# Performance work log

Measured on AMD Instinct MI355X. Metric: run time of the kernel, lower is better.

## Reference

```python
import jax, jax.numpy as jnp
import numpy as np

EMBED_DIM = 1024
N_HEADS = 16
HEAD_DIM = EMBED_DIM // N_HEADS
B, T = 1, 4096

def setup_inputs() -> dict:
    key = jax.random.key(0)
    k1, k2, k3 = jax.random.split(key, 3)
    x = jax.random.normal(k1, (B, T, EMBED_DIM), dtype=jnp.float32)
    # match nn.Linear init scale roughly (not required for correctness testing)
    w_qkv = jax.random.normal(k2, (EMBED_DIM, 3 * EMBED_DIM), dtype=jnp.float32) * (EMBED_DIM ** -0.5)
    w_out = jax.random.normal(k3, (EMBED_DIM, EMBED_DIM), dtype=jnp.float32) * (EMBED_DIM ** -0.5)
    return {"x": x, "w_qkv": w_qkv, "w_out": w_out}

def reference(x, w_qkv, w_out):
    b, t, c = x.shape
    qkv = x @ w_qkv                                  # [B,T,3C]
    q, k, v = jnp.split(qkv, 3, axis=-1)
    # [B,T,C] -> [B,H,T,D]
    def heads(a):
        return a.reshape(b, t, N_HEADS, HEAD_DIM).transpose(0, 2, 1, 3)
    q, k, v = heads(q), heads(k), heads(v)
    scale = 1.0 / jnp.sqrt(jnp.asarray(HEAD_DIM, dtype=x.dtype))
    att = jnp.einsum('bhqd,bhkd->bhqk', q, k) * scale  # [B,H,T,T] (full matrix, as in source)
    att = jax.nn.softmax(att, axis=-1)
    y = jnp.einsum('bhqk,bhkd->bhqd', att, v)          # [B,H,T,D]
    y = y.transpose(0, 2, 1, 3).reshape(b, t, c)
    return y @ w_out
```

## Files before the change

kernel.cpp:

```cpp
#include <hip/hip_runtime.h>
#include <hip/hip_bf16.h>

#define T_SEQ 4096
#define C_DIM 1024
#define NH    16
#define HD    64
#define C3    3072

typedef __attribute__((ext_vector_type(8))) short short8;
typedef __attribute__((ext_vector_type(4))) short short4v;
typedef __attribute__((ext_vector_type(4))) float f32x4;
typedef __attribute__((ext_vector_type(16))) float f32x16;

__device__ __forceinline__ short f2bf(float f) {
  union { float f; unsigned u; } v; v.f = f;
  unsigned r = v.u + 0x7FFFu + ((v.u >> 16) & 1u);
  return (short)(r >> 16);
}

__device__ __forceinline__ unsigned cvt_pk_bf16(float lo, float hi) {
  unsigned r;
  asm volatile("v_cvt_pk_bf16_f32 %0, %1, %2" : "=v"(r) : "v"(lo), "v"(hi));
  return r;
}

__device__ __forceinline__ float exp2_fast(float x) {
  return __builtin_amdgcn_exp2f(x);
}

__device__ __forceinline__ float max_half64(float v) {
  return fmaxf(v, __shfl_xor(v, 32, 64));
}
__device__ __forceinline__ float sum_half64(float v) {
  return v + __shfl_xor(v, 32, 64);
}

__device__ __forceinline__ void gld_lds16(const void* g, void* l) {
  __builtin_amdgcn_global_load_lds(
      (const __attribute__((address_space(1))) unsigned int*)g,
      (__attribute__((address_space(3))) unsigned int*)l, 16, 0, 0);
}

__global__ __launch_bounds__(256) void conv_bf16_kernel(const float* __restrict__ in,
                                                        short* __restrict__ out) {
  const size_t i = ((size_t)blockIdx.x * 256 + threadIdx.x) * 8;
  float4 v0 = *(const float4*)(in + i);
  float4 v1 = *(const float4*)(in + i + 4);
  short8 o;
  o[0] = f2bf(v0.x); o[1] = f2bf(v0.y); o[2] = f2bf(v0.z); o[3] = f2bf(v0.w);
  o[4] = f2bf(v1.x); o[5] = f2bf(v1.y); o[6] = f2bf(v1.z); o[7] = f2bf(v1.w);
  *(short8*)(out + i) = o;
}

__global__ void trans_conv_kernel(const float* __restrict__ in, short* __restrict__ out,
                                  int K, int N) {
  __shared__ float t[32][33];
  const int n0 = blockIdx.x * 32, k0 = blockIdx.y * 32;
  const int tx = threadIdx.x, ty = threadIdx.y;
  for (int i = ty; i < 32; i += 8) t[i][tx] = in[(size_t)(k0 + i) * N + n0 + tx];
  __syncthreads();
  for (int i = ty; i < 32; i += 8) out[(size_t)(n0 + i) * K + k0 + tx] = f2bf(t[tx][i]);
}

__device__ __forceinline__ void store_out(short* C, size_t idx, float v) { C[idx] = f2bf(v); }
__device__ __forceinline__ void store_out(float* C, size_t idx, float v) { C[idx] = v; }

template <typename OutT>
__global__ __launch_bounds__(256) void gemm_bt_kernel(const short* __restrict__ A,
                                                      const short* __restrict__ BT,
                                                      OutT* __restrict__ C,
                                                      int M, int N, int K) {
  __shared__ __align__(16) short As[128 * 32];
  __shared__ __align__(16) short Bs[128 * 32];
  const int tid = threadIdx.x;
  const int wid = tid >> 6;
  const int lane = tid & 63;
  const int l15 = lane & 15;
  const int l4 = lane >> 4;
  const int wr = wid >> 1;
  const int wc = wid & 1;
  const int bm = blockIdx.y * 128;
  const int bn = blockIdx.x * 128;

  f32x4 acc[4][4];
#pragma unroll
  for (int m = 0; m < 4; ++m)
#pragma unroll
    for (int n = 0; n < 4; ++n) acc[m][n] = (f32x4){0.f, 0.f, 0.f, 0.f};

  const int ebase = wid * 1024;
  const int e0 = ebase + lane * 8;
  const int r0 = e0 >> 5, c0 = e0 & 31;
  const int r1 = r0 + 16;

  for (int k0 = 0; k0 < K; k0 += 32) {
    __syncthreads();
    gld_lds16(A + (size_t)(bm + r0) * K + k0 + c0, As + ebase);
    gld_lds16(A + (size_t)(bm + r1) * K + k0 + c0, As + ebase + 512);
    gld_lds16(BT + (size_t)(bn + r0) * K + k0 + c0, Bs + ebase);
    gld_lds16(BT + (size_t)(bn + r1) * K + k0 + c0, Bs + ebase + 512);
    __syncthreads();

    short8 a[4], b[4];
#pragma unroll
    for (int m = 0; m < 4; ++m)
      a[m] = *(const short8*)&As[(wr * 64 + m * 16 + l15) * 32 + l4 * 8];
#pragma unroll
    for (int n = 0; n < 4; ++n)
      b[n] = *(const short8*)&Bs[(wc * 64 + n * 16 + l15) * 32 + l4 * 8];
#pragma unroll
    for (int m = 0; m < 4; ++m)
#pragma unroll
      for (int n = 0; n < 4; ++n)
        acc[m][n] = __builtin_amdgcn_mfma_f32_16x16x32_bf16(a[m], b[n], acc[m][n], 0, 0, 0);
  }

#pragma unroll
  for (int m = 0; m < 4; ++m) {
    const int row0 = bm + wr * 64 + m * 16 + l4 * 4;
#pragma unroll
    for (int n = 0; n < 4; ++n) {
      const int col = bn + wc * 64 + n * 16 + l15;
#pragma unroll
      for (int r = 0; r < 4; ++r)
        store_out(C, (size_t)(row0 + r) * N + col, acc[m][n][r]);
    }
  }
}

__global__ __launch_bounds__(256) void repack_v_kernel(const short* __restrict__ qkv,
                                                       short* __restrict__ vT) {
  const int h = blockIdx.x >> 6;
  const int t0 = (blockIdx.x & 63) << 6;
  __shared__ __align__(16) short tile[64][72];
  const int t = threadIdx.x;
  const int r = t >> 3, c = (t & 7) << 3;
#pragma unroll
  for (int i = 0; i < 2; ++i) {
    const int rr = r + i * 32;
    *(short8*)&tile[rr][c] =
        *(const short8*)&qkv[(size_t)(t0 + rr) * C3 + 2048 + h * 64 + c];
  }
  __syncthreads();
  const int d = t >> 3, tt = (t & 7) << 3;
#pragma unroll
  for (int i = 0; i < 2; ++i) {
    const int dd = d + i * 32;
    short8 v;
#pragma unroll
    for (int j = 0; j < 8; ++j) v[j] = tile[tt + j][dd];
    *(short8*)&vT[(size_t)(h * 64 + dd) * T_SEQ + t0 + tt] = v;
  }
}

__global__ __launch_bounds__(512, 4) void attn_kernel(const short* __restrict__ qkv,
                                                      const short* __restrict__ vT,
                                                      short* __restrict__ y) {
  const int bid = blockIdx.x;
  const int xcd = bid & 7, slot = bid >> 3;
  const int h = xcd * 2 + (slot >> 5);
  const int q0 = (slot & 31) * 128;

  const int tid = threadIdx.x;
  const int w = tid >> 6, lane = tid & 63, l31 = lane & 31, l1 = lane >> 5;
  const int g = w >> 2, wg = w & 3;
  const int kvbase = g * (T_SEQ / 2);

  __shared__ __align__(16) short Ks[2][2][4096];
  __shared__ __align__(16) short Vs[2][2][4096];

  short8 qf[4];
  {
    const short* qp = qkv + (size_t)(q0 + wg * 32 + l31) * C3 + h * 64 + l1 * 8;
#pragma unroll
    for (int ks = 0; ks < 4; ++ks) qf[ks] = *(const short8*)(qp + ks * 16);
  }

  f32x16 oa0, oa1;
#pragma unroll
  for (int r = 0; r < 16; ++r) { oa0[r] = 0.f; oa1[r] = 0.f; }
  float m_r = -INFINITY, l_r = 0.f;
  const float SCL = 0.125f * 1.44269504f;
  const float TH = 8.0f / SCL;

  const int lr0 = wg * 8 + (lane >> 3);
  const int csw = ((lane & 7) << 3) ^ ((lane >> 3) << 3);
  const short* kgb = qkv + 1024 + h * 64 + csw;
  const short* vgb = vT + (size_t)(h * 64 + lr0) * T_SEQ + csw;
  const int rswz = (l31 & 7) << 3;

  auto stage = [&](int buf, int kv0) {
#pragma unroll
    for (int i = 0; i < 2; ++i) {
      gld_lds16(kgb + (size_t)(kv0 + lr0 + i * 32) * C3, &Ks[g][buf][i * 2048 + wg * 512]);
      gld_lds16(vgb + (size_t)(i * 32) * T_SEQ + kv0, &Vs[g][buf][i * 2048 + wg * 512]);
    }
  };

  stage(0, kvbase);

  const int NT = T_SEQ / 2 / 64;
  for (int t = 0; t < NT; ++t) {
    const int cur = t & 1;
    __syncthreads();
    if (t < NT - 1) stage(cur ^ 1, kvbase + (t + 1) * 64);

    const short* Kb = &Ks[g][cur][0];
    const short* Vb = &Vs[g][cur][0];

    f32x16 s0, s1;
#pragma unroll
    for (int r = 0; r < 16; ++r) { s0[r] = 0.f; s1[r] = 0.f; }
    __builtin_amdgcn_s_setprio(1);
#pragma unroll
    for (int ks = 0; ks < 4; ++ks) {
      const int c = (ks * 16 + l1 * 8) ^ rswz;
      short8 k0 = *(const short8*)&Kb[l31 * 64 + c];
      short8 k1 = *(const short8*)&Kb[(32 + l31) * 64 + c];
      s0 = __builtin_amdgcn_mfma_f32_32x32x16_bf16(k0, qf[ks], s0, 0, 0, 0);
      s1 = __builtin_amdgcn_mfma_f32_32x32x16_bf16(k1, qf[ks], s1, 0, 0, 0);
    }
    __builtin_amdgcn_s_setprio(0);

    float tm;
    {
      float t8[8];
#pragma unroll
      for (int r = 0; r < 8; ++r)
        t8[r] = fmaxf(fmaxf(s0[r], s0[r + 8]), fmaxf(s1[r], s1[r + 8]));
#pragma unroll
      for (int r = 0; r < 4; ++r) t8[r] = fmaxf(t8[r], t8[r + 4]);
      tm = fmaxf(fmaxf(t8[0], t8[2]), fmaxf(t8[1], t8[3]));
    }
    tm = max_half64(tm);

    if (__any(tm > m_r + TH)) {
      const float mn = fmaxf(m_r, tm);
      const float al = exp2_fast((m_r - mn) * SCL);
      m_r = mn;
      l_r *= al;
#pragma unroll
      for (int r = 0; r < 16; ++r) { oa0[r] *= al; oa1[r] *= al; }
    }
    const float msc = m_r * SCL;
#pragma unroll
    for (int r = 0; r < 16; ++r) s0[r] = exp2_fast(fmaf(s0[r], SCL, -msc));
#pragma unroll
    for (int r = 0; r < 16; ++r) s1[r] = exp2_fast(fmaf(s1[r], SCL, -msc));

    float ps;
    {
      float u8[8];
#pragma unroll
      for (int r = 0; r < 8; ++r)
        u8[r] = (s0[r] + s0[r + 8]) + (s1[r] + s1[r + 8]);
#pragma unroll
      for (int r = 0; r < 4; ++r) u8[r] += u8[r + 4];
      ps = (u8[0] + u8[2]) + (u8[1] + u8[3]);
    }
    ps = sum_half64(ps);
    l_r += ps;

    unsigned pw[4][4];
#pragma unroll
    for (int half = 0; half < 2; ++half) {
      const f32x16& sv = half ? s1 : s0;
#pragma unroll
      for (int kk = 0; kk < 2; ++kk) {
        const int ks = half * 2 + kk;
        unsigned x0 = cvt_pk_bf16(sv[kk * 8 + 0], sv[kk * 8 + 1]);
        unsigned y0 = cvt_pk_bf16(sv[kk * 8 + 4], sv[kk * 8 + 5]);
        asm volatile("s_nop 0\n\tv_permlane32_swap_b32 %0, %1" : "+v"(x0), "+v"(y0));
        unsigned x1 = cvt_pk_bf16(sv[kk * 8 + 2], sv[kk * 8 + 3]);
        unsigned y1 = cvt_pk_bf16(sv[kk * 8 + 6], sv[kk * 8 + 7]);
        asm volatile("s_nop 0\n\tv_permlane32_swap_b32 %0, %1" : "+v"(x1), "+v"(y1));
        pw[ks][0] = x0; pw[ks][1] = x1; pw[ks][2] = y0; pw[ks][3] = y1;
      }
    }

    __builtin_amdgcn_s_setprio(1);
#pragma unroll
    for (int ks = 0; ks < 4; ++ks) {
      union { unsigned u[4]; short8 s8; } uu;
      uu.u[0] = pw[ks][0]; uu.u[1] = pw[ks][1]; uu.u[2] = pw[ks][2]; uu.u[3] = pw[ks][3];
      const int c = (ks * 16 + l1 * 8) ^ rswz;
      short8 v0 = *(const short8*)&Vb[l31 * 64 + c];
      short8 v1 = *(const short8*)&Vb[(32 + l31) * 64 + c];
      oa0 = __builtin_amdgcn_mfma_f32_32x32x16_bf16(v0, uu.s8, oa0, 0, 0, 0);
      oa1 = __builtin_amdgcn_mfma_f32_32x32x16_bf16(v1, uu.s8, oa1, 0, 0, 0);
    }
    __builtin_amdgcn_s_setprio(0);
  }

  __syncthreads();
  float* Oex = (float*)&Vs[0][0][0];
  float* mex = (float*)&Ks[0][0][0];
  const int xslot = wg * 64 + lane;
  if (g == 1) {
#pragma unroll
    for (int r = 0; r < 16; ++r) {
      Oex[r * 256 + xslot] = oa0[r];
      Oex[(16 + r) * 256 + xslot] = oa1[r];
    }
    mex[xslot] = m_r;
    mex[256 + xslot] = l_r;
  }
  __syncthreads();
  if (g == 0) {
    const float m_b = mex[xslot], l_b = mex[256 + xslot];
    const float mm = fmaxf(m_r, m_b);
    const float a = exp2_fast((m_r - mm) * SCL);
    const float b = exp2_fast((m_b - mm) * SCL);
    const float rl = 1.0f / (l_r * a + l_b * b);
    const float ra = a * rl, rb = b * rl;
    const size_t yb = (size_t)(q0 + wg * 32 + l31) * C_DIM + h * 64;
#pragma unroll
    for (int g4 = 0; g4 < 4; ++g4) {
      short4v o0, o1;
#pragma unroll
      for (int j = 0; j < 4; ++j) {
        o0[j] = f2bf(oa0[g4 * 4 + j] * ra + Oex[(g4 * 4 + j) * 256 + xslot] * rb);
        o1[j] = f2bf(oa1[g4 * 4 + j] * ra + Oex[(16 + g4 * 4 + j) * 256 + xslot] * rb);
      }
      *(short4v*)&y[yb + g4 * 8 + l1 * 4] = o0;
      *(short4v*)&y[yb + 32 + g4 * 8 + l1 * 4] = o1;
    }
  }
}

extern "C" void kernel_launch(void* const* d_in, const int* in_sizes, int n_in,
                              void* d_out, int out_size, void* d_ws, size_t ws_size,
                              hipStream_t stream) {
  const float* x = (const float*)d_in[0];
  const float* w_qkv = (const float*)d_in[1];
  const float* w_out = (const float*)d_in[2];
  float* out = (float*)d_out;

  char* ws = (char*)d_ws;
  short* xb = (short*)ws;            ws += (size_t)T_SEQ * C_DIM * 2;
  short* wqT = (short*)ws;           ws += (size_t)C3 * C_DIM * 2;
  short* woT = (short*)ws;           ws += (size_t)C_DIM * C_DIM * 2;
  short* qkv = (short*)ws;           ws += (size_t)T_SEQ * C3 * 2;
  short* vT = (short*)ws;            ws += (size_t)NH * T_SEQ * HD * 2;
  short* y = (short*)ws;             ws += (size_t)T_SEQ * C_DIM * 2;

  conv_bf16_kernel<<<(T_SEQ * C_DIM) / (256 * 8), 256, 0, stream>>>(x, xb);
  trans_conv_kernel<<<dim3(C3 / 32, C_DIM / 32), dim3(32, 8), 0, stream>>>(w_qkv, wqT, C_DIM, C3);
  trans_conv_kernel<<<dim3(C_DIM / 32, C_DIM / 32), dim3(32, 8), 0, stream>>>(w_out, woT, C_DIM, C_DIM);

  gemm_bt_kernel<short><<<dim3(C3 / 128, T_SEQ / 128), 256, 0, stream>>>(xb, wqT, qkv,
                                                                         T_SEQ, C3, C_DIM);
  repack_v_kernel<<<NH * (T_SEQ / 64), 256, 0, stream>>>(qkv, vT);

  attn_kernel<<<512, 512, 0, stream>>>(qkv, vT, y);

  gemm_bt_kernel<float><<<dim3(C_DIM / 128, T_SEQ / 128), 256, 0, stream>>>(y, woT, out,
                                                                            T_SEQ, C_DIM, C_DIM);
}
```

Baseline: 182.3 us.

## Pipeline KV staging with explicit vmcnt waits and split barriers

Replaces the single __syncthreads with two raw s_barriers around the next-tile prefetch, and waits with vmcnt(4) so only the current tile's async global-to-LDS loads must land while the next tile's stay in flight. K/V global pointers are now advanced incrementally instead of recomputed each iteration. The row-max reduction is restructured into 3-input max groups so the compiler can emit v_max3. The hand-written waitcnt relies on exact load counting, and any miscount would cause an LDS race.

```diff
diff --git a/kernel.cpp b/kernel.cpp
--- a/kernel.cpp
+++ b/kernel.cpp
@@ -33,6 +33,10 @@
 }
 __device__ __forceinline__ float sum_half64(float v) {
   return v + __shfl_xor(v, 32, 64);
+}
+
+__device__ __forceinline__ float m3(float a, float b, float c) {
+  return fmaxf(fmaxf(a, b), c);
 }
 
 __device__ __forceinline__ void gld_lds16(const void* g, void* l) {
@@ -185,25 +189,35 @@
 
   const int lr0 = wg * 8 + (lane >> 3);
   const int csw = ((lane & 7) << 3) ^ ((lane >> 3) << 3);
-  const short* kgb = qkv + 1024 + h * 64 + csw;
-  const short* vgb = vT + (size_t)(h * 64 + lr0) * T_SEQ + csw;
+  const short* kpt = qkv + 1024 + h * 64 + csw + (size_t)(kvbase + lr0) * C3;
+  const short* vpt = vT + (size_t)(h * 64 + lr0) * T_SEQ + csw + kvbase;
   const int rswz = (l31 & 7) << 3;
 
-  auto stage = [&](int buf, int kv0) {
+  auto stage = [&](int buf) {
 #pragma unroll
     for (int i = 0; i < 2; ++i) {
-      gld_lds16(kgb + (size_t)(kv0 + lr0 + i * 32) * C3, &Ks[g][buf][i * 2048 + wg * 512]);
-      gld_lds16(vgb + (size_t)(i * 32) * T_SEQ + kv0, &Vs[g][buf][i * 2048 + wg * 512]);
+      gld_lds16(kpt + (size_t)i * 32 * C3, &Ks[g][buf][i * 2048 + wg * 512]);
+      gld_lds16(vpt + (size_t)i * 32 * T_SEQ, &Vs[g][buf][i * 2048 + wg * 512]);
     }
   };
 
-  stage(0, kvbase);
+  stage(0);
+  kpt += (size_t)64 * C3;
+  vpt += 64;
 
   const int NT = T_SEQ / 2 / 64;
   for (int t = 0; t < NT; ++t) {
     const int cur = t & 1;
-    __syncthreads();
-    if (t < NT - 1) stage(cur ^ 1, kvbase + (t + 1) * 64);
+    __builtin_amdgcn_s_barrier();
+    if (t + 1 < NT) {
+      stage(cur ^ 1);
+      kpt += (size_t)64 * C3;
+      vpt += 64;
+      asm volatile("s_waitcnt vmcnt(4)" ::: "memory");
+    } else {
+      asm volatile("s_waitcnt vmcnt(0)" ::: "memory");
+    }
+    __builtin_amdgcn_s_barrier();
 
     const short* Kb = &Ks[g][cur][0];
     const short* Vb = &Vs[g][cur][0];
@@ -224,13 +238,22 @@
 
     float tm;
     {
-      float t8[8];
-#pragma unroll
-      for (int r = 0; r < 8; ++r)
-        t8[r] = fmaxf(fmaxf(s0[r], s0[r + 8]), fmaxf(s1[r], s1[r + 8]));
-#pragma unroll
-      for (int r = 0; r < 4; ++r) t8[r] = fmaxf(t8[r], t8[r + 4]);
-      tm = fmaxf(fmaxf(t8[0], t8[2]), fmaxf(t8[1], t8[3]));
+      float v0 = m3(s0[0], s0[1], s0[2]);
+      float v1 = m3(s0[3], s0[4], s0[5]);
+      float v2 = m3(s0[6], s0[7], s0[8]);
+      float v3 = m3(s0[9], s0[10], s0[11]);
+      float v4 = m3(s0[12], s0[13], s0[14]);
+      float v5 = fmaxf(s0[15], s1[0]);
+      float v6 = m3(s1[1], s1[2], s1[3]);
+      float v7 = m3(s1[4], s1[5], s1[6]);
+      float v8 = m3(s1[7], s1[8], s1[9]);
+      float v9 = m3(s1[10], s1[11], s1[12]);
+      float v10 = m3(s1[13], s1[14], s1[15]);
+      float w0 = m3(v0, v1, v2);
+      float w1 = m3(v3, v4, v5);
+      float w2 = m3(v6, v7, v8);
+      float w3 = fmaxf(v9, v10);
+      tm = fmaxf(m3(w0, w1, w2), w3);
     }
     tm = max_half64(tm);
 
```

After: 180.0 us. Within noise of the previous version (-1.3%).

## Pre-pack K and V into MFMA fragment layout and stream directly to registers

Applied to the files above, without the earlier changes.

Replaces the V transpose kernel with two packing kernels that lay K and V out in the exact per-lane MFMA operand order in 32-key tiles. The attention kernel drops its LDS double buffering and barriers, and instead loads K/V fragments straight from global memory into registers, prefetching the next tile during softmax. Each tile now covers 32 keys, with a single S MFMA chain, and the row-sum shuffle is deferred to the end. This removes LDS traffic and per-tile synchronisation at the cost of more global/L2 loads and less latency hiding per step.

```diff
diff --git a/kernel.cpp b/kernel.cpp
--- a/kernel.cpp
+++ b/kernel.cpp
@@ -31,8 +31,9 @@
 __device__ __forceinline__ float max_half64(float v) {
   return fmaxf(v, __shfl_xor(v, 32, 64));
 }
-__device__ __forceinline__ float sum_half64(float v) {
-  return v + __shfl_xor(v, 32, 64);
+
+__device__ __forceinline__ float m3(float a, float b, float c) {
+  return fmaxf(fmaxf(a, b), c);
 }
 
 __device__ __forceinline__ void gld_lds16(const void* g, void* l) {
@@ -128,33 +129,43 @@
   }
 }
 
-__global__ __launch_bounds__(256) void repack_v_kernel(const short* __restrict__ qkv,
-                                                       short* __restrict__ vT) {
-  const int h = blockIdx.x >> 6;
-  const int t0 = (blockIdx.x & 63) << 6;
-  __shared__ __align__(16) short tile[64][72];
-  const int t = threadIdx.x;
-  const int r = t >> 3, c = (t & 7) << 3;
-#pragma unroll
-  for (int i = 0; i < 2; ++i) {
-    const int rr = r + i * 32;
-    *(short8*)&tile[rr][c] =
-        *(const short8*)&qkv[(size_t)(t0 + rr) * C3 + 2048 + h * 64 + c];
-  }
-  __syncthreads();
-  const int d = t >> 3, tt = (t & 7) << 3;
-#pragma unroll
-  for (int i = 0; i < 2; ++i) {
-    const int dd = d + i * 32;
-    short8 v;
-#pragma unroll
-    for (int j = 0; j < 8; ++j) v[j] = tile[tt + j][dd];
-    *(short8*)&vT[(size_t)(h * 64 + dd) * T_SEQ + t0 + tt] = v;
-  }
+__global__ __launch_bounds__(256) void pack_k_kernel(const short* __restrict__ qkv,
+                                                     short* __restrict__ pk) {
+  const int h = blockIdx.x >> 7, t = blockIdx.x & 127;
+  __shared__ __align__(16) short tile[32][72];
+  const int tid = threadIdx.x;
+  const int r = tid >> 3, c = (tid & 7) * 8;
+  *(short8*)&tile[r][c] =
+      *(const short8*)&qkv[(size_t)(t * 32 + r) * C3 + 1024 + h * 64 + c];
+  __syncthreads();
+  const int ks = tid >> 6, l = tid & 63;
+  short8 o;
+#pragma unroll
+  for (int j = 0; j < 8; ++j) o[j] = tile[l & 31][ks * 16 + ((l >> 5) * 8) + j];
+  *(short8*)&pk[(size_t)(((h * 128 + t) * 4 + ks)) * 512 + l * 8] = o;
+}
+
+__global__ __launch_bounds__(256) void pack_v_kernel(const short* __restrict__ qkv,
+                                                     short* __restrict__ pv) {
+  const int h = blockIdx.x >> 7, t = blockIdx.x & 127;
+  __shared__ __align__(16) short tile[32][72];
+  const int tid = threadIdx.x;
+  const int r = tid >> 3, c = (tid & 7) * 8;
+  *(short8*)&tile[r][c] =
+      *(const short8*)&qkv[(size_t)(t * 32 + r) * C3 + 2048 + h * 64 + c];
+  __syncthreads();
+  const int f = tid >> 6, l = tid & 63;
+  const int kh = f >> 1, dh = f & 1;
+  short8 o;
+#pragma unroll
+  for (int j = 0; j < 8; ++j)
+    o[j] = tile[kh * 16 + ((l >> 5) * 8) + j][(l & 31) + 32 * dh];
+  *(short8*)&pv[(size_t)(((h * 128 + t) * 4 + f)) * 512 + l * 8] = o;
 }
 
 __global__ __launch_bounds__(512, 4) void attn_kernel(const short* __restrict__ qkv,
-                                                      const short* __restrict__ vT,
+                                                      const short* __restrict__ pk,
+                                                      const short* __restrict__ pv,
                                                       short* __restrict__ y) {
   const int bid = blockIdx.x;
   const int xcd = bid & 7, slot = bid >> 3;
@@ -164,10 +175,9 @@
   const int tid = threadIdx.x;
   const int w = tid >> 6, lane = tid & 63, l31 = lane & 31, l1 = lane >> 5;
   const int g = w >> 2, wg = w & 3;
-  const int kvbase = g * (T_SEQ / 2);
-
-  __shared__ __align__(16) short Ks[2][2][4096];
-  __shared__ __align__(16) short Vs[2][2][4096];
+
+  __shared__ __align__(16) float Oex[32 * 256];
+  __shared__ float mex[512];
 
   short8 qf[4];
   {
@@ -183,59 +193,46 @@
   const float SCL = 0.125f * 1.44269504f;
   const float TH = 8.0f / SCL;
 
-  const int lr0 = wg * 8 + (lane >> 3);
-  const int csw = ((lane & 7) << 3) ^ ((lane >> 3) << 3);
-  const short* kgb = qkv + 1024 + h * 64 + csw;
-  const short* vgb = vT + (size_t)(h * 64 + lr0) * T_SEQ + csw;
-  const int rswz = (l31 & 7) << 3;
-
-  auto stage = [&](int buf, int kv0) {
-#pragma unroll
-    for (int i = 0; i < 2; ++i) {
-      gld_lds16(kgb + (size_t)(kv0 + lr0 + i * 32) * C3, &Ks[g][buf][i * 2048 + wg * 512]);
-      gld_lds16(vgb + (size_t)(i * 32) * T_SEQ + kv0, &Vs[g][buf][i * 2048 + wg * 512]);
-    }
-  };
-
-  stage(0, kvbase);
-
-  const int NT = T_SEQ / 2 / 64;
+  const short* kp = pk + ((size_t)(h * 128 + g * 64) * 4) * 512 + lane * 8;
+  const short* vp = pv + ((size_t)(h * 128 + g * 64) * 4) * 512 + lane * 8;
+
+  const int NT = 64;
+  short8 kf[4], vf[4];
+#pragma unroll
+  for (int f = 0; f < 4; ++f) kf[f] = *(const short8*)(kp + f * 512);
+#pragma unroll
+  for (int f = 0; f < 4; ++f) vf[f] = *(const short8*)(vp + f * 512);
+
   for (int t = 0; t < NT; ++t) {
-    const int cur = t & 1;
-    __syncthreads();
-    if (t < NT - 1) stage(cur ^ 1, kvbase + (t + 1) * 64);
-
-    const short* Kb = &Ks[g][cur][0];
-    const short* Vb = &Vs[g][cur][0];
-
-    f32x16 s0, s1;
-#pragma unroll
-    for (int r = 0; r < 16; ++r) { s0[r] = 0.f; s1[r] = 0.f; }
+    f32x16 s;
+#pragma unroll
+    for (int r = 0; r < 16; ++r) s[r] = 0.f;
     __builtin_amdgcn_s_setprio(1);
 #pragma unroll
-    for (int ks = 0; ks < 4; ++ks) {
-      const int c = (ks * 16 + l1 * 8) ^ rswz;
-      short8 k0 = *(const short8*)&Kb[l31 * 64 + c];
-      short8 k1 = *(const short8*)&Kb[(32 + l31) * 64 + c];
-      s0 = __builtin_amdgcn_mfma_f32_32x32x16_bf16(k0, qf[ks], s0, 0, 0, 0);
-      s1 = __builtin_amdgcn_mfma_f32_32x32x16_bf16(k1, qf[ks], s1, 0, 0, 0);
-    }
+    for (int ks = 0; ks < 4; ++ks)
+      s = __builtin_amdgcn_mfma_f32_32x32x16_bf16(kf[ks], qf[ks], s, 0, 0, 0);
     __builtin_amdgcn_s_setprio(0);
+
+    {
+      const int tn = (t + 1 < NT) ? t + 1 : t;
+      const short* kpn = kp + (size_t)tn * 2048;
+#pragma unroll
+      for (int f = 0; f < 4; ++f) kf[f] = *(const short8*)(kpn + f * 512);
+    }
 
     float tm;
     {
-      float t8[8];
-#pragma unroll
-      for (int r = 0; r < 8; ++r)
-        t8[r] = fmaxf(fmaxf(s0[r], s0[r + 8]), fmaxf(s1[r], s1[r + 8]));
-#pragma unroll
-      for (int r = 0; r < 4; ++r) t8[r] = fmaxf(t8[r], t8[r + 4]);
-      tm = fmaxf(fmaxf(t8[0], t8[2]), fmaxf(t8[1], t8[3]));
-    }
-    tm = max_half64(tm);
+      float v0 = m3(s[0], s[1], s[2]);
+      float v1 = m3(s[3], s[4], s[5]);
+      float v2 = m3(s[6], s[7], s[8]);
+      float v3 = m3(s[9], s[10], s[11]);
+      float v4 = m3(s[12], s[13], s[14]);
+      tm = fmaxf(m3(v0, v1, v2), m3(v3, v4, s[15]));
+    }
 
     if (__any(tm > m_r + TH)) {
-      const float mn = fmaxf(m_r, tm);
+      const float tmx = max_half64(tm);
+      const float mn = fmaxf(m_r, tmx);
       const float al = exp2_fast((m_r - mn) * SCL);
       m_r = mn;
       l_r *= al;
@@ -244,57 +241,50 @@
     }
     const float msc = m_r * SCL;
 #pragma unroll
-    for (int r = 0; r < 16; ++r) s0[r] = exp2_fast(fmaf(s0[r], SCL, -msc));
-#pragma unroll
-    for (int r = 0; r < 16; ++r) s1[r] = exp2_fast(fmaf(s1[r], SCL, -msc));
-
-    float ps;
+    for (int r = 0; r < 16; ++r) s[r] = exp2_fast(fmaf(s[r], SCL, -msc));
+
     {
-      float u8[8];
-#pragma unroll
-      for (int r = 0; r < 8; ++r)
-        u8[r] = (s0[r] + s0[r + 8]) + (s1[r] + s1[r + 8]);
-#pragma unroll
-      for (int r = 0; r < 4; ++r) u8[r] += u8[r + 4];
-      ps = (u8[0] + u8[2]) + (u8[1] + u8[3]);
-    }
-    ps = sum_half64(ps);
-    l_r += ps;
-
-    unsigned pw[4][4];
-#pragma unroll
-    for (int half = 0; half < 2; ++half) {
-      const f32x16& sv = half ? s1 : s0;
-#pragma unroll
-      for (int kk = 0; kk < 2; ++kk) {
-        const int ks = half * 2 + kk;
-        unsigned x0 = cvt_pk_bf16(sv[kk * 8 + 0], sv[kk * 8 + 1]);
-        unsigned y0 = cvt_pk_bf16(sv[kk * 8 + 4], sv[kk * 8 + 5]);
-        asm volatile("s_nop 0\n\tv_permlane32_swap_b32 %0, %1" : "+v"(x0), "+v"(y0));
-        unsigned x1 = cvt_pk_bf16(sv[kk * 8 + 2], sv[kk * 8 + 3]);
-        unsigned y1 = cvt_pk_bf16(sv[kk * 8 + 6], sv[kk * 8 + 7]);
-        asm volatile("s_nop 0\n\tv_permlane32_swap_b32 %0, %1" : "+v"(x1), "+v"(y1));
-        pw[ks][0] = x0; pw[ks][1] = x1; pw[ks][2] = y0; pw[ks][3] = y1;
-      }
+      float u[8];
+#pragma unroll
+      for (int r = 0; r < 8; ++r) u[r] = s[r] + s[r + 8];
+#pragma unroll
+      for (int r = 0; r < 4; ++r) u[r] += u[r + 4];
+      l_r += (u[0] + u[2]) + (u[1] + u[3]);
+    }
+
+    unsigned pw[2][4];
+#pragma unroll
+    for (int kh = 0; kh < 2; ++kh) {
+      unsigned x0 = cvt_pk_bf16(s[kh * 8 + 0], s[kh * 8 + 1]);
+      unsigned y0 = cvt_pk_bf16(s[kh * 8 + 4], s[kh * 8 + 5]);
+      asm volatile("s_nop 0\n\tv_permlane32_swap_b32 %0, %1" : "+v"(x0), "+v"(y0));
+      unsigned x1 = cvt_pk_bf16(s[kh * 8 + 2], s[kh * 8 + 3]);
+      unsigned y1 = cvt_pk_bf16(s[kh * 8 + 6], s[kh * 8 + 7]);
+      asm volatile("s_nop 0\n\tv_permlane32_swap_b32 %0, %1" : "+v"(x1), "+v"(y1));
+      pw[kh][0] = x0; pw[kh][1] = x1; pw[kh][2] = y0; pw[kh][3] = y1;
     }
 
     __builtin_amdgcn_s_setprio(1);
 #pragma unroll
-    for (int ks = 0; ks < 4; ++ks) {
+    for (int kh = 0; kh < 2; ++kh) {
       union { unsigned u[4]; short8 s8; } uu;
-      uu.u[0] = pw[ks][0]; uu.u[1] = pw[ks][1]; uu.u[2] = pw[ks][2]; uu.u[3] = pw[ks][3];
-      const int c = (ks * 16 + l1 * 8) ^ rswz;
-      short8 v0 = *(const short8*)&Vb[l31 * 64 + c];
-      short8 v1 = *(const short8*)&Vb[(32 + l31) * 64 + c];
-      oa0 = __builtin_amdgcn_mfma_f32_32x32x16_bf16(v0, uu.s8, oa0, 0, 0, 0);
-      oa1 = __builtin_amdgcn_mfma_f32_32x32x16_bf16(v1, uu.s8, oa1, 0, 0, 0);
+      uu.u[0] = pw[kh][0]; uu.u[1] = pw[kh][1]; uu.u[2] = pw[kh][2]; uu.u[3] = pw[kh][3];
+      oa0 = __builtin_amdgcn_mfma_f32_32x32x16_bf16(vf[kh * 2 + 0], uu.s8, oa0, 0, 0, 0);
+      oa1 = __builtin_amdgcn_mfma_f32_32x32x16_bf16(vf[kh * 2 + 1], uu.s8, oa1, 0, 0, 0);
     }
     __builtin_amdgcn_s_setprio(0);
-  }
-
-  __syncthreads();
-  float* Oex = (float*)&Vs[0][0][0];
-  float* mex = (float*)&Ks[0][0][0];
+
+    {
+      const int tn = (t + 1 < NT) ? t + 1 : t;
+      const short* vpn = vp + (size_t)tn * 2048;
+#pragma unroll
+      for (int f = 0; f < 4; ++f) vf[f] = *(const short8*)(vpn + f * 512);
+    }
+  }
+
+  l_r += __shfl_xor(l_r, 32, 64);
+
+  __syncthreads();
   const int xslot = wg * 64 + lane;
   if (g == 1) {
 #pragma unroll
@@ -341,8 +331,9 @@
   short* wqT = (short*)ws;           ws += (size_t)C3 * C_DIM * 2;
   short* woT = (short*)ws;           ws += (size_t)C_DIM * C_DIM * 2;
   short* qkv = (short*)ws;           ws += (size_t)T_SEQ * C3 * 2;
-  short* vT = (short*)ws;            ws += (size_t)NH * T_SEQ * HD * 2;
   short* y = (short*)ws;             ws += (size_t)T_SEQ * C_DIM * 2;
+  short* pk = (short*)ws;            ws += (size_t)NH * T_SEQ * HD * 2;
+  short* pv = (short*)ws;            ws += (size_t)NH * T_SEQ * HD * 2;
 
   conv_bf16_kernel<<<(T_SEQ * C_DIM) / (256 * 8), 256, 0, stream>>>(x, xb);
   trans_conv_kernel<<<dim3(C3 / 32, C_DIM / 32), dim3(32, 8), 0, stream>>>(w_qkv, wqT, C_DIM, C3);
@@ -350,9 +341,10 @@
 
   gemm_bt_kernel<short><<<dim3(C3 / 128, T_SEQ / 128), 256, 0, stream>>>(xb, wqT, qkv,
                                                                          T_SEQ, C3, C_DIM);
-  repack_v_kernel<<<NH * (T_SEQ / 64), 256, 0, stream>>>(qkv, vT);
-
-  attn_kernel<<<512, 512, 0, stream>>>(qkv, vT, y);
+  pack_k_kernel<<<NH * 128, 256, 0, stream>>>(qkv, pk);
+  pack_v_kernel<<<NH * 128, 256, 0, stream>>>(qkv, pv);
+
+  attn_kernel<<<512, 512, 0, stream>>>(qkv, pk, pv, y);
 
   gemm_bt_kernel<float><<<dim3(C_DIM / 128, T_SEQ / 128), 256, 0, stream>>>(y, woT, out,
                                                                             T_SEQ, C_DIM, C_DIM);
```

After: 187.4 us. 1.03x slower.

## Software-pipeline QK^T one tile ahead with split K/V staging in attention

Applied to the files above, without the earlier changes.

Restructures the attention loop so the QK^T MFMAs for tile t+1 run while softmax and PV for tile t execute, and K and V loads are staged separately, with K two tiles ahead. Raw s_waitcnt plus s_barrier replace __syncthreads. The row max now uses a 3-input max tree and does its cross-half shuffle only inside the rescale branch. The row-sum shuffle is deferred to a single one after the loop. Drops the occupancy hint from launch bounds and the setprio calls. This adds a second score accumulator set, raising register pressure.

```diff
diff --git a/kernel.cpp b/kernel.cpp
--- a/kernel.cpp
+++ b/kernel.cpp
@@ -31,8 +31,9 @@
 __device__ __forceinline__ float max_half64(float v) {
   return fmaxf(v, __shfl_xor(v, 32, 64));
 }
-__device__ __forceinline__ float sum_half64(float v) {
-  return v + __shfl_xor(v, 32, 64);
+
+__device__ __forceinline__ float m3(float a, float b, float c) {
+  return fmaxf(fmaxf(a, b), c);
 }
 
 __device__ __forceinline__ void gld_lds16(const void* g, void* l) {
@@ -153,9 +154,9 @@
   }
 }
 
-__global__ __launch_bounds__(512, 4) void attn_kernel(const short* __restrict__ qkv,
-                                                      const short* __restrict__ vT,
-                                                      short* __restrict__ y) {
+__global__ __launch_bounds__(512) void attn_kernel(const short* __restrict__ qkv,
+                                                   const short* __restrict__ vT,
+                                                   short* __restrict__ y) {
   const int bid = blockIdx.x;
   const int xcd = bid & 7, slot = bid >> 3;
   const int h = xcd * 2 + (slot >> 5);
@@ -185,57 +186,79 @@
 
   const int lr0 = wg * 8 + (lane >> 3);
   const int csw = ((lane & 7) << 3) ^ ((lane >> 3) << 3);
-  const short* kgb = qkv + 1024 + h * 64 + csw;
-  const short* vgb = vT + (size_t)(h * 64 + lr0) * T_SEQ + csw;
+  const short* kgb = qkv + 1024 + h * 64 + csw + (size_t)(kvbase + lr0) * C3;
+  const short* vgb = vT + (size_t)(h * 64 + lr0) * T_SEQ + csw + kvbase;
   const int rswz = (l31 & 7) << 3;
 
-  auto stage = [&](int buf, int kv0) {
-#pragma unroll
-    for (int i = 0; i < 2; ++i) {
-      gld_lds16(kgb + (size_t)(kv0 + lr0 + i * 32) * C3, &Ks[g][buf][i * 2048 + wg * 512]);
-      gld_lds16(vgb + (size_t)(i * 32) * T_SEQ + kv0, &Vs[g][buf][i * 2048 + wg * 512]);
-    }
+  auto stageK = [&](int sl, int tt) {
+#pragma unroll
+    for (int i = 0; i < 2; ++i)
+      gld_lds16(kgb + (size_t)(tt * 64 + i * 32) * C3, &Ks[g][sl][i * 2048 + wg * 512]);
   };
-
-  stage(0, kvbase);
-
-  const int NT = T_SEQ / 2 / 64;
-  for (int t = 0; t < NT; ++t) {
-    const int cur = t & 1;
-    __syncthreads();
-    if (t < NT - 1) stage(cur ^ 1, kvbase + (t + 1) * 64);
-
-    const short* Kb = &Ks[g][cur][0];
-    const short* Vb = &Vs[g][cur][0];
-
-    f32x16 s0, s1;
-#pragma unroll
-    for (int r = 0; r < 16; ++r) { s0[r] = 0.f; s1[r] = 0.f; }
-    __builtin_amdgcn_s_setprio(1);
+  auto stageV = [&](int sl, int tt) {
+#pragma unroll
+    for (int i = 0; i < 2; ++i)
+      gld_lds16(vgb + (size_t)(i * 32) * T_SEQ + tt * 64, &Vs[g][sl][i * 2048 + wg * 512]);
+  };
+
+  auto QK = [&](int sl, f32x16& sa, f32x16& sb) {
+    const short* Kb = &Ks[g][sl][0];
 #pragma unroll
     for (int ks = 0; ks < 4; ++ks) {
       const int c = (ks * 16 + l1 * 8) ^ rswz;
       short8 k0 = *(const short8*)&Kb[l31 * 64 + c];
       short8 k1 = *(const short8*)&Kb[(32 + l31) * 64 + c];
-      s0 = __builtin_amdgcn_mfma_f32_32x32x16_bf16(k0, qf[ks], s0, 0, 0, 0);
-      s1 = __builtin_amdgcn_mfma_f32_32x32x16_bf16(k1, qf[ks], s1, 0, 0, 0);
-    }
-    __builtin_amdgcn_s_setprio(0);
+      sa = __builtin_amdgcn_mfma_f32_32x32x16_bf16(k0, qf[ks], sa, 0, 0, 0);
+      sb = __builtin_amdgcn_mfma_f32_32x32x16_bf16(k1, qf[ks], sb, 0, 0, 0);
+    }
+  };
+
+  stageK(0, 0);
+  stageV(0, 0);
+  stageK(1, 1);
+  asm volatile("s_waitcnt vmcnt(2)" ::: "memory");
+  __builtin_amdgcn_s_barrier();
+
+  f32x16 sP0, sP1;
+#pragma unroll
+  for (int r = 0; r < 16; ++r) { sP0[r] = 0.f; sP1[r] = 0.f; }
+  QK(0, sP0, sP1);
+
+  const int NT = T_SEQ / 2 / 64;
+  for (int t = 0; t < NT; ++t) {
+    asm volatile("s_waitcnt vmcnt(0)" ::: "memory");
+    __builtin_amdgcn_s_barrier();
+
+    if (t + 2 < NT) stageK(t & 1, t + 2);
+    if (t + 1 < NT) stageV((t + 1) & 1, t + 1);
+
+    f32x16 sN0, sN1;
+#pragma unroll
+    for (int r = 0; r < 16; ++r) { sN0[r] = 0.f; sN1[r] = 0.f; }
+    if (t + 1 < NT) QK((t + 1) & 1, sN0, sN1);
 
     float tm;
     {
-      float t8[8];
-#pragma unroll
-      for (int r = 0; r < 8; ++r)
-        t8[r] = fmaxf(fmaxf(s0[r], s0[r + 8]), fmaxf(s1[r], s1[r + 8]));
-#pragma unroll
-      for (int r = 0; r < 4; ++r) t8[r] = fmaxf(t8[r], t8[r + 4]);
-      tm = fmaxf(fmaxf(t8[0], t8[2]), fmaxf(t8[1], t8[3]));
-    }
-    tm = max_half64(tm);
-
+      float v0 = m3(sP0[0], sP0[1], sP0[2]);
+      float v1 = m3(sP0[3], sP0[4], sP0[5]);
+      float v2 = m3(sP0[6], sP0[7], sP0[8]);
+      float v3 = m3(sP0[9], sP0[10], sP0[11]);
+      float v4 = m3(sP0[12], sP0[13], sP0[14]);
+      float v5 = fmaxf(sP0[15], sP1[0]);
+      float v6 = m3(sP1[1], sP1[2], sP1[3]);
+      float v7 = m3(sP1[4], sP1[5], sP1[6]);
+      float v8 = m3(sP1[7], sP1[8], sP1[9]);
+      float v9 = m3(sP1[10], sP1[11], sP1[12]);
+      float v10 = m3(sP1[13], sP1[14], sP1[15]);
+      float w0 = m3(v0, v1, v2);
+      float w1 = m3(v3, v4, v5);
+      float w2 = m3(v6, v7, v8);
+      float w3 = fmaxf(v9, v10);
+      tm = fmaxf(m3(w0, w1, w2), w3);
+    }
     if (__any(tm > m_r + TH)) {
-      const float mn = fmaxf(m_r, tm);
+      const float tmx = max_half64(tm);
+      const float mn = fmaxf(m_r, tmx);
       const float al = exp2_fast((m_r - mn) * SCL);
       m_r = mn;
       l_r *= al;
@@ -244,27 +267,23 @@
     }
     const float msc = m_r * SCL;
 #pragma unroll
-    for (int r = 0; r < 16; ++r) s0[r] = exp2_fast(fmaf(s0[r], SCL, -msc));
-#pragma unroll
-    for (int r = 0; r < 16; ++r) s1[r] = exp2_fast(fmaf(s1[r], SCL, -msc));
-
-    float ps;
+    for (int r = 0; r < 16; ++r) sP0[r] = exp2_fast(fmaf(sP0[r], SCL, -msc));
+#pragma unroll
+    for (int r = 0; r < 16; ++r) sP1[r] = exp2_fast(fmaf(sP1[r], SCL, -msc));
+
     {
-      float u8[8];
-#pragma unroll
-      for (int r = 0; r < 8; ++r)
-        u8[r] = (s0[r] + s0[r + 8]) + (s1[r] + s1[r + 8]);
-#pragma unroll
-      for (int r = 0; r < 4; ++r) u8[r] += u8[r + 4];
-      ps = (u8[0] + u8[2]) + (u8[1] + u8[3]);
-    }
-    ps = sum_half64(ps);
-    l_r += ps;
+      float u[8];
+#pragma unroll
+      for (int r = 0; r < 8; ++r) u[r] = (sP0[r] + sP0[r + 8]) + (sP1[r] + sP1[r + 8]);
+#pragma unroll
+      for (int r = 0; r < 4; ++r) u[r] += u[r + 4];
+      l_r += (u[0] + u[2]) + (u[1] + u[3]);
+    }
 
     unsigned pw[4][4];
 #pragma unroll
     for (int half = 0; half < 2; ++half) {
-      const f32x16& sv = half ? s1 : s0;
+      const f32x16& sv = half ? sP1 : sP0;
 #pragma unroll
       for (int kk = 0; kk < 2; ++kk) {
         const int ks = half * 2 + kk;
@@ -278,19 +297,25 @@
       }
     }
 
-    __builtin_amdgcn_s_setprio(1);
-#pragma unroll
-    for (int ks = 0; ks < 4; ++ks) {
-      union { unsigned u[4]; short8 s8; } uu;
-      uu.u[0] = pw[ks][0]; uu.u[1] = pw[ks][1]; uu.u[2] = pw[ks][2]; uu.u[3] = pw[ks][3];
-      const int c = (ks * 16 + l1 * 8) ^ rswz;
-      short8 v0 = *(const short8*)&Vb[l31 * 64 + c];
-      short8 v1 = *(const short8*)&Vb[(32 + l31) * 64 + c];
-      oa0 = __builtin_amdgcn_mfma_f32_32x32x16_bf16(v0, uu.s8, oa0, 0, 0, 0);
-      oa1 = __builtin_amdgcn_mfma_f32_32x32x16_bf16(v1, uu.s8, oa1, 0, 0, 0);
-    }
-    __builtin_amdgcn_s_setprio(0);
-  }
+    {
+      const short* Vb = &Vs[g][t & 1][0];
+#pragma unroll
+      for (int ks = 0; ks < 4; ++ks) {
+        union { unsigned u[4]; short8 s8; } uu;
+        uu.u[0] = pw[ks][0]; uu.u[1] = pw[ks][1]; uu.u[2] = pw[ks][2]; uu.u[3] = pw[ks][3];
+        const int c = (ks * 16 + l1 * 8) ^ rswz;
+        short8 v0 = *(const short8*)&Vb[l31 * 64 + c];
+        short8 v1 = *(const short8*)&Vb[(32 + l31) * 64 + c];
+        oa0 = __builtin_amdgcn_mfma_f32_32x32x16_bf16(v0, uu.s8, oa0, 0, 0, 0);
+        oa1 = __builtin_amdgcn_mfma_f32_32x32x16_bf16(v1, uu.s8, oa1, 0, 0, 0);
+      }
+    }
+
+    sP0 = sN0;
+    sP1 = sN1;
+  }
+
+  l_r += __shfl_xor(l_r, 32, 64);
 
   __syncthreads();
   float* Oex = (float*)&Vs[0][0][0];
```

Measured after the change: 196.5 us. +7.8%, slower.
